# Kernel optimization log

Measured on AMD Instinct MI355X. Metric: run time of the kernel, lower is better.

## Reference

```python
import jax, jax.numpy as jnp
import numpy as np

N = 100000
E = 1600000
IN_DIM = 128
OUT_DIM = 128
K = 2
LN_EPS = 1e-5


def setup_inputs() -> dict:
    key = jax.random.key(0)
    k1, k2, k3, k4 = jax.random.split(key, 4)
    x = jax.random.normal(k1, (N, IN_DIM), dtype=jnp.float32)
    edge_index = jax.random.randint(k2, (2, E), 0, N, dtype=jnp.int64)
    # LayerNorm params (elementwise affine, torch defaults)
    ln_w = jnp.ones((IN_DIM,), dtype=jnp.float32)
    ln_b = jnp.zeros((IN_DIM,), dtype=jnp.float32)
    # SGConv linear params (torch nn.Linear layout: [out, in])
    bound = 1.0 / np.sqrt(IN_DIM)
    W = jax.random.uniform(k3, (OUT_DIM, IN_DIM), minval=-bound, maxval=bound, dtype=jnp.float32)
    b = jax.random.uniform(k4, (OUT_DIM,), minval=-bound, maxval=bound, dtype=jnp.float32)
    return {"x": x, "edge_index": edge_index, "ln_w": ln_w, "ln_b": ln_b, "W": W, "b": b}


def _layer_norm(x, w, b):
    mu = jnp.mean(x, axis=-1, keepdims=True)
    var = jnp.mean(jnp.square(x - mu), axis=-1, keepdims=True)
    return (x - mu) * jax.lax.rsqrt(var + LN_EPS) * w + b


def _sgc_propagate(x, edge_index):
    # gcn_norm with added self-loops: A_hat = D^{-1/2} (A + I) D^{-1/2}
    src, dst = edge_index[0], edge_index[1]
    loop = jnp.arange(N, dtype=src.dtype)
    src_a = jnp.concatenate([src, loop])
    dst_a = jnp.concatenate([dst, loop])
    deg = jax.ops.segment_sum(jnp.ones((E + N,), dtype=x.dtype), dst_a, num_segments=N)
    dinv = jnp.where(deg > 0, jax.lax.rsqrt(jnp.maximum(deg, 1e-12)), 0.0)
    w = dinv[src_a] * dinv[dst_a]  # [E+N]
    for _ in range(K):
        x = jax.ops.segment_sum(x[src_a] * w[:, None], dst_a, num_segments=N)
    return x


def reference(x, edge_index, ln_w, ln_b, W, b):
    y = _layer_norm(x, ln_w, ln_b)
    y = _sgc_propagate(y, edge_index)
    return y @ W.T + b
```

## Files before the change

kernel.cpp:

```cpp
#include <hip/hip_runtime.h>
#include <hip/hip_fp16.h>

#define DIM 128
#define BKT_SHIFT 8
#define BKT_NODES 256
#define CHUNK 8192
#define MAXBUK 1024

typedef _Float16 half8 __attribute__((ext_vector_type(8)));
typedef float f32x4 __attribute__((ext_vector_type(4)));


__global__ __launch_bounds__(256) void k_s1_hist(const int* __restrict__ ei, int* __restrict__ H,
                                                 int E, int NBUK, int NBLK) {
    __shared__ int hist[MAXBUK];
    int b = blockIdx.x, tid = threadIdx.x;
    for (int i = tid; i < NBUK; i += 256) hist[i] = 0;
    __syncthreads();
    int e0 = b * CHUNK, e1 = min(e0 + CHUNK, E);
    for (int e = e0 + tid; e < e1; e += 256) {
        int dst = ei[E + e];
        atomicAdd(&hist[dst >> BKT_SHIFT], 1);
    }
    __syncthreads();
    for (int k = tid; k < NBUK; k += 256) H[(size_t)k * NBLK + b] = hist[k];
}


__global__ __launch_bounds__(256) void k_scanA(const int* __restrict__ in, int* __restrict__ tmp,
                                               int* __restrict__ bsum, int n) {
    __shared__ int s[256];
    int tid = threadIdx.x;
    int i = blockIdx.x * 256 + tid;
    int v = (i < n) ? in[i] : 0;
    s[tid] = v;
    __syncthreads();
    for (int off = 1; off < 256; off <<= 1) {
        int t = (tid >= off) ? s[tid - off] : 0;
        __syncthreads();
        s[tid] += t;
        __syncthreads();
    }
    if (i < n) tmp[i] = s[tid];
    if (tid == 255) bsum[blockIdx.x] = s[255];
}

__global__ __launch_bounds__(1024) void k_scanB(int* __restrict__ bsum, int nb) {
    __shared__ int s[1024];
    int tid = threadIdx.x;
    int v = (tid < nb) ? bsum[tid] : 0;
    s[tid] = v;
    __syncthreads();
    for (int off = 1; off < 1024; off <<= 1) {
        int t = (tid >= off) ? s[tid - off] : 0;
        __syncthreads();
        s[tid] += t;
        __syncthreads();
    }
    if (tid < nb) bsum[tid] = s[tid] - v;
}

__global__ __launch_bounds__(256) void k_scanE(int* __restrict__ H, const int* __restrict__ tmp,
                                               const int* __restrict__ bsum, int n) {
    int i = blockIdx.x * 256 + threadIdx.x;
    if (i < n) H[i] = bsum[blockIdx.x] + tmp[i] - H[i];
}


__global__ __launch_bounds__(256) void k_s3_scatter(const int* __restrict__ ei,
                                                    const int* __restrict__ H,
                                                    int* __restrict__ ssrc,
                                                    unsigned char* __restrict__ sdst, int E,
                                                    int NBUK, int NBLK) {
    __shared__ int off[MAXBUK];
    int b = blockIdx.x, tid = threadIdx.x;
    for (int k = tid; k < NBUK; k += 256) off[k] = H[(size_t)k * NBLK + b];
    __syncthreads();
    int e0 = b * CHUNK, e1 = min(e0 + CHUNK, E);
    for (int e = e0 + tid; e < e1; e += 256) {
        int src = ei[e];
        int dst = ei[E + e];
        int p = atomicAdd(&off[dst >> BKT_SHIFT], 1);
        ssrc[p] = src;
        sdst[p] = (unsigned char)(dst & (BKT_NODES - 1));
    }
}


__global__ __launch_bounds__(256) void k_s4_build(const int* __restrict__ H,
                                                  const int* __restrict__ ssrc,
                                                  const unsigned char* __restrict__ sdst,
                                                  int* __restrict__ rp, float* __restrict__ dinv,
                                                  int* __restrict__ col, int N, int E, int NBUK,
                                                  int NBLK) {
    __shared__ int cnt[BKT_NODES];
    __shared__ int pos[BKT_NODES];
    __shared__ int s[BKT_NODES];
    int bkt = blockIdx.x, tid = threadIdx.x;
    int base = H[(size_t)bkt * NBLK];
    int endv = (bkt + 1 < NBUK) ? H[(size_t)(bkt + 1) * NBLK] : E;
    int m = endv - base;
    cnt[tid] = 0;
    __syncthreads();
    for (int i = tid; i < m; i += 256) atomicAdd(&cnt[sdst[base + i]], 1);
    __syncthreads();
    int v = cnt[tid];
    s[tid] = v;
    __syncthreads();
    for (int off = 1; off < 256; off <<= 1) {
        int t = (tid >= off) ? s[tid - off] : 0;
        __syncthreads();
        s[tid] += t;
        __syncthreads();
    }
    int excl = s[tid] - v;
    pos[tid] = excl;
    int node = bkt * BKT_NODES + tid;
    if (node < N) {
        rp[node] = base + excl;
        dinv[node] = rsqrtf((float)(v + 1));
    }
    __syncthreads();
    for (int i = tid; i < m; i += 256) {
        int r = atomicAdd(&pos[sdst[base + i]], 1);
        col[base + r] = ssrc[base + i];
    }
    if (bkt == 0 && tid == 0) rp[N] = E;
}


__global__ __launch_bounds__(256) void k_ln(const float* __restrict__ x,
                                            const float* __restrict__ w,
                                            const float* __restrict__ bb,
                                            const float* __restrict__ dinv,
                                            __half2* __restrict__ u, int N) {
    int row = (blockIdx.x * 256 + threadIdx.x) >> 6;
    int lane = threadIdx.x & 63;
    if (row >= N) return;
    float2 v = *(const float2*)(x + (size_t)row * DIM + lane * 2);
    float s = v.x + v.y;
#pragma unroll
    for (int o = 32; o; o >>= 1) s += __shfl_xor(s, o, 64);
    float mu = s * (1.0f / 128.0f);
    float dx0 = v.x - mu, dx1 = v.y - mu;
    float ss = dx0 * dx0 + dx1 * dx1;
#pragma unroll
    for (int o = 32; o; o >>= 1) ss += __shfl_xor(ss, o, 64);
    float rs = rsqrtf(ss * (1.0f / 128.0f) + 1e-5f);
    float2 wv = *(const float2*)(w + lane * 2);
    float2 bv = *(const float2*)(bb + lane * 2);
    float di = dinv[row];
    float o0 = (dx0 * rs * wv.x + bv.x) * di;
    float o1 = (dx1 * rs * wv.y + bv.y) * di;
    u[(size_t)row * 64 + lane] = __floats2half2_rn(o0, o1);
}


__global__ __launch_bounds__(256) void k_prop(const _Float16* __restrict__ X,
                                              _Float16* __restrict__ Y,
                                              const int* __restrict__ rp,
                                              const int* __restrict__ col,
                                              const float* __restrict__ dinv, int N, int squared) {
    int tid = threadIdx.x;
    int node = blockIdx.x * 16 + (tid >> 4);
    int q = tid & 15;
    if (node >= N) return;
    const _Float16* xq = X + q * 8;
    half8 selfv = *(const half8*)(xq + (size_t)node * DIM);
    int e0 = rp[node], e1 = rp[node + 1];
    float acc[8];
#pragma unroll
    for (int f = 0; f < 8; f++) acc[f] = 0.f;
    int e = e0;
    for (; e + 7 < e1; e += 8) {
        int s0 = col[e + 0], s1 = col[e + 1], s2 = col[e + 2], s3 = col[e + 3];
        int s4 = col[e + 4], s5 = col[e + 5], s6 = col[e + 6], s7 = col[e + 7];
        half8 g0 = *(const half8*)(xq + (size_t)s0 * DIM);
        half8 g1 = *(const half8*)(xq + (size_t)s1 * DIM);
        half8 g2 = *(const half8*)(xq + (size_t)s2 * DIM);
        half8 g3 = *(const half8*)(xq + (size_t)s3 * DIM);
        half8 g4 = *(const half8*)(xq + (size_t)s4 * DIM);
        half8 g5 = *(const half8*)(xq + (size_t)s5 * DIM);
        half8 g6 = *(const half8*)(xq + (size_t)s6 * DIM);
        half8 g7 = *(const half8*)(xq + (size_t)s7 * DIM);
#pragma unroll
        for (int f = 0; f < 8; f++)
            acc[f] += (((float)g0[f] + (float)g1[f]) + ((float)g2[f] + (float)g3[f])) +
                      (((float)g4[f] + (float)g5[f]) + ((float)g6[f] + (float)g7[f]));
    }
    for (; e + 1 < e1; e += 2) {
        int s0 = col[e], s1 = col[e + 1];
        half8 g0 = *(const half8*)(xq + (size_t)s0 * DIM);
        half8 g1 = *(const half8*)(xq + (size_t)s1 * DIM);
#pragma unroll
        for (int f = 0; f < 8; f++) acc[f] += (float)g0[f] + (float)g1[f];
    }
    if (e < e1) {
        int s = col[e];
        half8 g = *(const half8*)(xq + (size_t)s * DIM);
#pragma unroll
        for (int f = 0; f < 8; f++) acc[f] += (float)g[f];
    }
    float di = dinv[node];
    float sc = squared ? di * di : di;
    half8 o;
#pragma unroll
    for (int f = 0; f < 8; f++) o[f] = (_Float16)(((float)selfv[f] + acc[f]) * sc);
    *(half8*)(Y + (size_t)node * DIM + q * 8) = o;
}


__global__ __launch_bounds__(256) void k_packW(const float* __restrict__ W,
                                               _Float16* __restrict__ pack) {
    int t = blockIdx.x * 256 + threadIdx.x;
    if (t >= 2048) return;
    int lane = t & 63, ks = (t >> 6) & 3, tile = t >> 8;
    int wrow = tile * 16 + (lane & 15);
    int wcol = ks * 32 + 8 * (lane >> 4);
    float4 w0 = *(const float4*)(W + wrow * DIM + wcol);
    float4 w1 = *(const float4*)(W + wrow * DIM + wcol + 4);
    _Float16* dst = pack + (size_t)t * 8;
    dst[0] = (_Float16)w0.x; dst[1] = (_Float16)w0.y;
    dst[2] = (_Float16)w0.z; dst[3] = (_Float16)w0.w;
    dst[4] = (_Float16)w1.x; dst[5] = (_Float16)w1.y;
    dst[6] = (_Float16)w1.z; dst[7] = (_Float16)w1.w;
}

__global__ __launch_bounds__(256) void k_mm(const _Float16* __restrict__ Z,
                                            const _Float16* __restrict__ pack,
                                            const float* __restrict__ bias,
                                            float* __restrict__ out, int N) {
    int wave = threadIdx.x >> 6;
    int lane = threadIdx.x & 63;
    int rB = blockIdx.x * 64 + wave * 16;
    int r = rB + (lane & 15);
    bool rok = (r < N);
    half8 a[4];
    if (rok) {
        const _Float16* zr = Z + (size_t)r * DIM + 8 * (lane >> 4);
#pragma unroll
        for (int ks = 0; ks < 4; ks++) a[ks] = *(const half8*)(zr + ks * 32);
    } else {
#pragma unroll
        for (int ks = 0; ks < 4; ks++)
#pragma unroll
            for (int j = 0; j < 8; j++) a[ks][j] = (_Float16)0;
    }
    int row0 = rB + (lane >> 4) * 4;
#pragma unroll
    for (int tile = 0; tile < 8; tile++) {
        f32x4 d = {0.f, 0.f, 0.f, 0.f};
#pragma unroll
        for (int ks = 0; ks < 4; ks++) {
            half8 bf = *(const half8*)(pack + ((size_t)((tile * 4 + ks) * 64 + lane)) * 8);
            d = __builtin_amdgcn_mfma_f32_16x16x32_f16(a[ks], bf, d, 0, 0, 0);
        }
        int c = tile * 16 + (lane & 15);
        float bv = bias[c];
#pragma unroll
        for (int j = 0; j < 4; j++) {
            int rr = row0 + j;
            if (rr < N) out[(size_t)rr * DIM + c] = d[j] + bv;
        }
    }
}


extern "C" void kernel_launch(void* const* d_in, const int* in_sizes, int n_in, void* d_out,
                              int out_size, void* d_ws, size_t ws_size, hipStream_t stream) {
    const float* x = (const float*)d_in[0];
    const int* ei = (const int*)d_in[1];
    const float* ln_w = (const float*)d_in[2];
    const float* ln_b = (const float*)d_in[3];
    const float* W = (const float*)d_in[4];
    const float* b = (const float*)d_in[5];
    float* out = (float*)d_out;

    int N = in_sizes[0] / DIM;
    int E = in_sizes[1] / 2;

    int NBUK = (N + BKT_NODES - 1) / BKT_NODES;
    int NBLK = (E + CHUNK - 1) / CHUNK;
    int M = NBUK * NBLK;
    int gScan = (M + 255) / 256;

    char* p = (char*)d_ws;
    auto carve = [&](size_t bytes) {
        void* r = (void*)p;
        p += (bytes + 255) & ~(size_t)255;
        return r;
    };
    __half* u0 = (__half*)carve((size_t)N * DIM * 2);
    __half* u1 = (__half*)carve((size_t)N * DIM * 2);
    _Float16* pack = (_Float16*)carve(DIM * DIM * 2);
    int* H = (int*)carve((size_t)M * 4);
    float* dinv = (float*)carve((size_t)N * 4);
    int* rp = (int*)carve((size_t)(N + 1) * 4);
    int* tmp = (int*)carve((size_t)(N > M ? N : M) * 4);
    int* bsum = (int*)carve(1024 * 4);
    int* col = (int*)carve((size_t)E * 4);

    int* ssrc = (int*)u1;
    unsigned char* sdst = (unsigned char*)u1 + ((size_t)E * 4 + 255 & ~(size_t)255);

    int gW = (N + 3) / 4;
    int gP = (N + 15) / 16;
    int gM = (N + 63) / 64;

    k_s1_hist<<<NBLK, 256, 0, stream>>>(ei, H, E, NBUK, NBLK);
    k_scanA<<<gScan, 256, 0, stream>>>(H, tmp, bsum, M);
    k_scanB<<<1, 1024, 0, stream>>>(bsum, gScan);
    k_scanE<<<gScan, 256, 0, stream>>>(H, tmp, bsum, M);
    k_s3_scatter<<<NBLK, 256, 0, stream>>>(ei, H, ssrc, sdst, E, NBUK, NBLK);
    k_s4_build<<<NBUK, 256, 0, stream>>>(H, ssrc, sdst, rp, dinv, col, N, E, NBUK, NBLK);
    k_packW<<<8, 256, 0, stream>>>(W, pack);
    k_ln<<<gW, 256, 0, stream>>>(x, ln_w, ln_b, dinv, (__half2*)u0, N);
    k_prop<<<gP, 256, 0, stream>>>((const _Float16*)u0, (_Float16*)u1, rp, col, dinv, N, 1);
    k_prop<<<gP, 256, 0, stream>>>((const _Float16*)u1, (_Float16*)u0, rp, col, dinv, N, 0);
    k_mm<<<gM, 256, 0, stream>>>((const _Float16*)u0, pack, b, out, N);
}
```

Before: 225.7 us.

## Fuse second propagation with output matmul via LDS tile; enlarge sort blocks

The second SpMM propagation is fused with the final linear layer. Each block aggregates 64 rows into a padded LDS tile and then runs MFMA on that tile, so the fp16 intermediate no longer makes a round trip through global memory and one launch is removed. The histogram and scatter kernels now use 1024-thread blocks on 4096-edge chunks, which gives more blocks and parallelism in preprocessing but also more atomic contention in LDS. Each fused block's four row groups run their gathers serially, which may lower memory-level parallelism compared with the separate prop kernel.

```diff
diff --git a/kernel.cpp b/kernel.cpp
--- a/kernel.cpp
+++ b/kernel.cpp
@@ -4,26 +4,27 @@
 #define DIM 128
 #define BKT_SHIFT 8
 #define BKT_NODES 256
-#define CHUNK 8192
+#define CHUNK 4096
 #define MAXBUK 1024
+#define ZROW 136
 
 typedef _Float16 half8 __attribute__((ext_vector_type(8)));
 typedef float f32x4 __attribute__((ext_vector_type(4)));
 
 
-__global__ __launch_bounds__(256) void k_s1_hist(const int* __restrict__ ei, int* __restrict__ H,
-                                                 int E, int NBUK, int NBLK) {
+__global__ __launch_bounds__(1024) void k_s1_hist(const int* __restrict__ ei, int* __restrict__ H,
+                                                  int E, int NBUK, int NBLK) {
     __shared__ int hist[MAXBUK];
     int b = blockIdx.x, tid = threadIdx.x;
-    for (int i = tid; i < NBUK; i += 256) hist[i] = 0;
+    for (int i = tid; i < NBUK; i += 1024) hist[i] = 0;
     __syncthreads();
     int e0 = b * CHUNK, e1 = min(e0 + CHUNK, E);
-    for (int e = e0 + tid; e < e1; e += 256) {
+    for (int e = e0 + tid; e < e1; e += 1024) {
         int dst = ei[E + e];
         atomicAdd(&hist[dst >> BKT_SHIFT], 1);
     }
     __syncthreads();
-    for (int k = tid; k < NBUK; k += 256) H[(size_t)k * NBLK + b] = hist[k];
+    for (int k = tid; k < NBUK; k += 1024) H[(size_t)k * NBLK + b] = hist[k];
 }
 
 
@@ -67,17 +68,17 @@
 }
 
 
-__global__ __launch_bounds__(256) void k_s3_scatter(const int* __restrict__ ei,
-                                                    const int* __restrict__ H,
-                                                    int* __restrict__ ssrc,
-                                                    unsigned char* __restrict__ sdst, int E,
-                                                    int NBUK, int NBLK) {
+__global__ __launch_bounds__(1024) void k_s3_scatter(const int* __restrict__ ei,
+                                                     const int* __restrict__ H,
+                                                     int* __restrict__ ssrc,
+                                                     unsigned char* __restrict__ sdst, int E,
+                                                     int NBUK, int NBLK) {
     __shared__ int off[MAXBUK];
     int b = blockIdx.x, tid = threadIdx.x;
-    for (int k = tid; k < NBUK; k += 256) off[k] = H[(size_t)k * NBLK + b];
+    for (int k = tid; k < NBUK; k += 1024) off[k] = H[(size_t)k * NBLK + b];
     __syncthreads();
     int e0 = b * CHUNK, e1 = min(e0 + CHUNK, E);
-    for (int e = e0 + tid; e < e1; e += 256) {
+    for (int e = e0 + tid; e < e1; e += 1024) {
         int src = ei[e];
         int dst = ei[E + e];
         int p = atomicAdd(&off[dst >> BKT_SHIFT], 1);
@@ -160,7 +161,7 @@
                                               _Float16* __restrict__ Y,
                                               const int* __restrict__ rp,
                                               const int* __restrict__ col,
-                                              const float* __restrict__ dinv, int N, int squared) {
+                                              const float* __restrict__ dinv, int N) {
     int tid = threadIdx.x;
     int node = blockIdx.x * 16 + (tid >> 4);
     int q = tid & 15;
@@ -202,7 +203,7 @@
         for (int f = 0; f < 8; f++) acc[f] += (float)g[f];
     }
     float di = dinv[node];
-    float sc = squared ? di * di : di;
+    float sc = di * di;
     half8 o;
 #pragma unroll
     for (int f = 0; f < 8; f++) o[f] = (_Float16)(((float)selfv[f] + acc[f]) * sc);
@@ -226,27 +227,79 @@
     dst[6] = (_Float16)w1.z; dst[7] = (_Float16)w1.w;
 }
 
-__global__ __launch_bounds__(256) void k_mm(const _Float16* __restrict__ Z,
-                                            const _Float16* __restrict__ pack,
-                                            const float* __restrict__ bias,
-                                            float* __restrict__ out, int N) {
-    int wave = threadIdx.x >> 6;
-    int lane = threadIdx.x & 63;
-    int rB = blockIdx.x * 64 + wave * 16;
-    int r = rB + (lane & 15);
-    bool rok = (r < N);
+
+__global__ __launch_bounds__(256) void k_prop_mm(const _Float16* __restrict__ X,
+                                                 const int* __restrict__ rp,
+                                                 const int* __restrict__ col,
+                                                 const float* __restrict__ dinv,
+                                                 const _Float16* __restrict__ pack,
+                                                 const float* __restrict__ bias,
+                                                 float* __restrict__ out, int N) {
+    __shared__ _Float16 Z[64 * ZROW];
+    int tid = threadIdx.x;
+    int rB = blockIdx.x * 64;
+    int g = tid >> 4;
+    int q = tid & 15;
+    const _Float16* xq = X + q * 8;
+#pragma unroll
+    for (int k = 0; k < 4; k++) {
+        int lrow = g * 4 + k;
+        int node = rB + lrow;
+        half8 o;
+        if (node < N) {
+            half8 selfv = *(const half8*)(xq + (size_t)node * DIM);
+            int e0 = rp[node], e1 = rp[node + 1];
+            float acc[8];
+#pragma unroll
+            for (int f = 0; f < 8; f++) acc[f] = 0.f;
+            int e = e0;
+            for (; e + 7 < e1; e += 8) {
+                int s0 = col[e + 0], s1 = col[e + 1], s2 = col[e + 2], s3 = col[e + 3];
+                int s4 = col[e + 4], s5 = col[e + 5], s6 = col[e + 6], s7 = col[e + 7];
+                half8 g0 = *(const half8*)(xq + (size_t)s0 * DIM);
+                half8 g1 = *(const half8*)(xq + (size_t)s1 * DIM);
+                half8 g2 = *(const half8*)(xq + (size_t)s2 * DIM);
+                half8 g3 = *(const half8*)(xq + (size_t)s3 * DIM);
+                half8 g4 = *(const half8*)(xq + (size_t)s4 * DIM);
+                half8 g5 = *(const half8*)(xq + (size_t)s5 * DIM);
+                half8 g6 = *(const half8*)(xq + (size_t)s6 * DIM);
+                half8 g7 = *(const half8*)(xq + (size_t)s7 * DIM);
+#pragma unroll
+                for (int f = 0; f < 8; f++)
+                    acc[f] += (((float)g0[f] + (float)g1[f]) + ((float)g2[f] + (float)g3[f])) +
+                              (((float)g4[f] + (float)g5[f]) + ((float)g6[f] + (float)g7[f]));
+            }
+            for (; e + 1 < e1; e += 2) {
+                int s0 = col[e], s1 = col[e + 1];
+                half8 g0 = *(const half8*)(xq + (size_t)s0 * DIM);
+                half8 g1 = *(const half8*)(xq + (size_t)s1 * DIM);
+#pragma unroll
+                for (int f = 0; f < 8; f++) acc[f] += (float)g0[f] + (float)g1[f];
+            }
+            if (e < e1) {
+                int s = col[e];
+                half8 gg = *(const half8*)(xq + (size_t)s * DIM);
+#pragma unroll
+                for (int f = 0; f < 8; f++) acc[f] += (float)gg[f];
+            }
+            float sc = dinv[node];
+#pragma unroll
+            for (int f = 0; f < 8; f++) o[f] = (_Float16)(((float)selfv[f] + acc[f]) * sc);
+        } else {
+#pragma unroll
+            for (int f = 0; f < 8; f++) o[f] = (_Float16)0;
+        }
+        *(half8*)(&Z[lrow * ZROW + q * 8]) = o;
+    }
+    __syncthreads();
+    int wave = tid >> 6;
+    int lane = tid & 63;
+    int rw = wave * 16;
     half8 a[4];
-    if (rok) {
-        const _Float16* zr = Z + (size_t)r * DIM + 8 * (lane >> 4);
-#pragma unroll
-        for (int ks = 0; ks < 4; ks++) a[ks] = *(const half8*)(zr + ks * 32);
-    } else {
-#pragma unroll
-        for (int ks = 0; ks < 4; ks++)
-#pragma unroll
-            for (int j = 0; j < 8; j++) a[ks][j] = (_Float16)0;
-    }
-    int row0 = rB + (lane >> 4) * 4;
+#pragma unroll
+    for (int ks = 0; ks < 4; ks++)
+        a[ks] = *(const half8*)(&Z[(rw + (lane & 15)) * ZROW + ks * 32 + (lane >> 4) * 8]);
+    int row0 = rB + rw + (lane >> 4) * 4;
 #pragma unroll
     for (int tile = 0; tile < 8; tile++) {
         f32x4 d = {0.f, 0.f, 0.f, 0.f};
@@ -307,15 +360,14 @@
     int gP = (N + 15) / 16;
     int gM = (N + 63) / 64;
 
-    k_s1_hist<<<NBLK, 256, 0, stream>>>(ei, H, E, NBUK, NBLK);
+    k_s1_hist<<<NBLK, 1024, 0, stream>>>(ei, H, E, NBUK, NBLK);
     k_scanA<<<gScan, 256, 0, stream>>>(H, tmp, bsum, M);
     k_scanB<<<1, 1024, 0, stream>>>(bsum, gScan);
     k_scanE<<<gScan, 256, 0, stream>>>(H, tmp, bsum, M);
-    k_s3_scatter<<<NBLK, 256, 0, stream>>>(ei, H, ssrc, sdst, E, NBUK, NBLK);
+    k_s3_scatter<<<NBLK, 1024, 0, stream>>>(ei, H, ssrc, sdst, E, NBUK, NBLK);
     k_s4_build<<<NBUK, 256, 0, stream>>>(H, ssrc, sdst, rp, dinv, col, N, E, NBUK, NBLK);
     k_packW<<<8, 256, 0, stream>>>(W, pack);
     k_ln<<<gW, 256, 0, stream>>>(x, ln_w, ln_b, dinv, (__half2*)u0, N);
-    k_prop<<<gP, 256, 0, stream>>>((const _Float16*)u0, (_Float16*)u1, rp, col, dinv, N, 1);
-    k_prop<<<gP, 256, 0, stream>>>((const _Float16*)u1, (_Float16*)u0, rp, col, dinv, N, 0);
-    k_mm<<<gM, 256, 0, stream>>>((const _Float16*)u0, pack, b, out, N);
-}
+    k_prop<<<gP, 256, 0, stream>>>((const _Float16*)u0, (_Float16*)u1, rp, col, dinv, N);
+    k_prop_mm<<<gM, 256, 0, stream>>>((const _Float16*)u1, rp, col, dinv, pack, b, out, N);
+}
```

Result: faster. 219.5 us (-2.7%).

## Pack edge src/dst into one word, fold scan fixup and W packing into build

Applied to the files above, without the earlier changes.

The separate scan-finalise kernel is removed: the exclusive offsets are now computed on the fly from the scan temporaries in the scatter and build kernels. Source and local destination are packed into one 32-bit word, so the sort stage uses a single store and load instead of an int array plus a byte array. W packing is merged into the build kernel as extra blocks. The histogram and scatter kernels now use 1024-thread blocks with smaller chunks. Together these cut launches and memory traffic in the CSR build, but they assume node ids fit in 17 bits.

```diff
diff --git a/kernel.cpp b/kernel.cpp
--- a/kernel.cpp
+++ b/kernel.cpp
@@ -4,26 +4,28 @@
 #define DIM 128
 #define BKT_SHIFT 8
 #define BKT_NODES 256
-#define CHUNK 8192
+#define CHUNK 4096
 #define MAXBUK 1024
+#define SRC_BITS 17
+#define SRC_MASK 0x1FFFF
 
 typedef _Float16 half8 __attribute__((ext_vector_type(8)));
 typedef float f32x4 __attribute__((ext_vector_type(4)));
 
 
-__global__ __launch_bounds__(256) void k_s1_hist(const int* __restrict__ ei, int* __restrict__ H,
-                                                 int E, int NBUK, int NBLK) {
+__global__ __launch_bounds__(1024) void k_s1_hist(const int* __restrict__ ei, int* __restrict__ H,
+                                                  int E, int NBUK, int NBLK) {
     __shared__ int hist[MAXBUK];
     int b = blockIdx.x, tid = threadIdx.x;
-    for (int i = tid; i < NBUK; i += 256) hist[i] = 0;
+    for (int i = tid; i < NBUK; i += 1024) hist[i] = 0;
     __syncthreads();
     int e0 = b * CHUNK, e1 = min(e0 + CHUNK, E);
-    for (int e = e0 + tid; e < e1; e += 256) {
+    for (int e = e0 + tid; e < e1; e += 1024) {
         int dst = ei[E + e];
         atomicAdd(&hist[dst >> BKT_SHIFT], 1);
     }
     __syncthreads();
-    for (int k = tid; k < NBUK; k += 256) H[(size_t)k * NBLK + b] = hist[k];
+    for (int k = tid; k < NBUK; k += 1024) H[(size_t)k * NBLK + b] = hist[k];
 }
 
 
@@ -60,49 +62,67 @@
     if (tid < nb) bsum[tid] = s[tid] - v;
 }
 
-__global__ __launch_bounds__(256) void k_scanE(int* __restrict__ H, const int* __restrict__ tmp,
-                                               const int* __restrict__ bsum, int n) {
-    int i = blockIdx.x * 256 + threadIdx.x;
-    if (i < n) H[i] = bsum[blockIdx.x] + tmp[i] - H[i];
-}
-
-
-__global__ __launch_bounds__(256) void k_s3_scatter(const int* __restrict__ ei,
-                                                    const int* __restrict__ H,
-                                                    int* __restrict__ ssrc,
-                                                    unsigned char* __restrict__ sdst, int E,
-                                                    int NBUK, int NBLK) {
+__device__ __forceinline__ int h_excl(const int* H, const int* tmp, const int* bsum, int i) {
+    return bsum[i >> 8] + tmp[i] - H[i];
+}
+
+
+__global__ __launch_bounds__(1024) void k_s3_scatter(const int* __restrict__ ei,
+                                                     const int* __restrict__ H,
+                                                     const int* __restrict__ tmp,
+                                                     const int* __restrict__ bsum,
+                                                     unsigned int* __restrict__ sedge, int E,
+                                                     int NBUK, int NBLK) {
     __shared__ int off[MAXBUK];
     int b = blockIdx.x, tid = threadIdx.x;
-    for (int k = tid; k < NBUK; k += 256) off[k] = H[(size_t)k * NBLK + b];
+    for (int k = tid; k < NBUK; k += 1024) {
+        int i = k * NBLK + b;
+        off[k] = h_excl(H, tmp, bsum, i);
+    }
     __syncthreads();
     int e0 = b * CHUNK, e1 = min(e0 + CHUNK, E);
-    for (int e = e0 + tid; e < e1; e += 256) {
+    for (int e = e0 + tid; e < e1; e += 1024) {
         int src = ei[e];
         int dst = ei[E + e];
         int p = atomicAdd(&off[dst >> BKT_SHIFT], 1);
-        ssrc[p] = src;
-        sdst[p] = (unsigned char)(dst & (BKT_NODES - 1));
+        sedge[p] = (unsigned int)src | ((unsigned int)(dst & (BKT_NODES - 1)) << SRC_BITS);
     }
 }
 
 
 __global__ __launch_bounds__(256) void k_s4_build(const int* __restrict__ H,
-                                                  const int* __restrict__ ssrc,
-                                                  const unsigned char* __restrict__ sdst,
+                                                  const int* __restrict__ tmp,
+                                                  const int* __restrict__ bsum,
+                                                  const unsigned int* __restrict__ sedge,
                                                   int* __restrict__ rp, float* __restrict__ dinv,
-                                                  int* __restrict__ col, int N, int E, int NBUK,
-                                                  int NBLK) {
+                                                  int* __restrict__ col,
+                                                  const float* __restrict__ W,
+                                                  _Float16* __restrict__ pack, int N, int E,
+                                                  int NBUK, int NBLK) {
+    int bkt = blockIdx.x, tid = threadIdx.x;
+    if (bkt >= NBUK) {
+        int t = (bkt - NBUK) * 256 + tid;
+        int lane = t & 63, ks = (t >> 6) & 3, tile = t >> 8;
+        int wrow = tile * 16 + (lane & 15);
+        int wcol = ks * 32 + 8 * (lane >> 4);
+        float4 w0 = *(const float4*)(W + wrow * DIM + wcol);
+        float4 w1 = *(const float4*)(W + wrow * DIM + wcol + 4);
+        _Float16* dst = pack + (size_t)t * 8;
+        dst[0] = (_Float16)w0.x; dst[1] = (_Float16)w0.y;
+        dst[2] = (_Float16)w0.z; dst[3] = (_Float16)w0.w;
+        dst[4] = (_Float16)w1.x; dst[5] = (_Float16)w1.y;
+        dst[6] = (_Float16)w1.z; dst[7] = (_Float16)w1.w;
+        return;
+    }
     __shared__ int cnt[BKT_NODES];
     __shared__ int pos[BKT_NODES];
     __shared__ int s[BKT_NODES];
-    int bkt = blockIdx.x, tid = threadIdx.x;
-    int base = H[(size_t)bkt * NBLK];
-    int endv = (bkt + 1 < NBUK) ? H[(size_t)(bkt + 1) * NBLK] : E;
+    int base = h_excl(H, tmp, bsum, bkt * NBLK);
+    int endv = (bkt + 1 < NBUK) ? h_excl(H, tmp, bsum, (bkt + 1) * NBLK) : E;
     int m = endv - base;
     cnt[tid] = 0;
     __syncthreads();
-    for (int i = tid; i < m; i += 256) atomicAdd(&cnt[sdst[base + i]], 1);
+    for (int i = tid; i < m; i += 256) atomicAdd(&cnt[sedge[base + i] >> SRC_BITS], 1);
     __syncthreads();
     int v = cnt[tid];
     s[tid] = v;
@@ -122,8 +142,9 @@
     }
     __syncthreads();
     for (int i = tid; i < m; i += 256) {
-        int r = atomicAdd(&pos[sdst[base + i]], 1);
-        col[base + r] = ssrc[base + i];
+        unsigned int ev = sedge[base + i];
+        int r = atomicAdd(&pos[ev >> SRC_BITS], 1);
+        col[base + r] = (int)(ev & SRC_MASK);
     }
     if (bkt == 0 && tid == 0) rp[N] = E;
 }
@@ -209,22 +230,6 @@
     *(half8*)(Y + (size_t)node * DIM + q * 8) = o;
 }
 
-
-__global__ __launch_bounds__(256) void k_packW(const float* __restrict__ W,
-                                               _Float16* __restrict__ pack) {
-    int t = blockIdx.x * 256 + threadIdx.x;
-    if (t >= 2048) return;
-    int lane = t & 63, ks = (t >> 6) & 3, tile = t >> 8;
-    int wrow = tile * 16 + (lane & 15);
-    int wcol = ks * 32 + 8 * (lane >> 4);
-    float4 w0 = *(const float4*)(W + wrow * DIM + wcol);
-    float4 w1 = *(const float4*)(W + wrow * DIM + wcol + 4);
-    _Float16* dst = pack + (size_t)t * 8;
-    dst[0] = (_Float16)w0.x; dst[1] = (_Float16)w0.y;
-    dst[2] = (_Float16)w0.z; dst[3] = (_Float16)w0.w;
-    dst[4] = (_Float16)w1.x; dst[5] = (_Float16)w1.y;
-    dst[6] = (_Float16)w1.z; dst[7] = (_Float16)w1.w;
-}
 
 __global__ __launch_bounds__(256) void k_mm(const _Float16* __restrict__ Z,
                                             const _Float16* __restrict__ pack,
@@ -300,20 +305,18 @@
     int* bsum = (int*)carve(1024 * 4);
     int* col = (int*)carve((size_t)E * 4);
 
-    int* ssrc = (int*)u1;
-    unsigned char* sdst = (unsigned char*)u1 + ((size_t)E * 4 + 255 & ~(size_t)255);
+    unsigned int* sedge = (unsigned int*)u1;
 
     int gW = (N + 3) / 4;
     int gP = (N + 15) / 16;
     int gM = (N + 63) / 64;
 
-    k_s1_hist<<<NBLK, 256, 0, stream>>>(ei, H, E, NBUK, NBLK);
+    k_s1_hist<<<NBLK, 1024, 0, stream>>>(ei, H, E, NBUK, NBLK);
     k_scanA<<<gScan, 256, 0, stream>>>(H, tmp, bsum, M);
     k_scanB<<<1, 1024, 0, stream>>>(bsum, gScan);
-    k_scanE<<<gScan, 256, 0, stream>>>(H, tmp, bsum, M);
-    k_s3_scatter<<<NBLK, 256, 0, stream>>>(ei, H, ssrc, sdst, E, NBUK, NBLK);
-    k_s4_build<<<NBUK, 256, 0, stream>>>(H, ssrc, sdst, rp, dinv, col, N, E, NBUK, NBLK);
-    k_packW<<<8, 256, 0, stream>>>(W, pack);
+    k_s3_scatter<<<NBLK, 1024, 0, stream>>>(ei, H, tmp, bsum, sedge, E, NBUK, NBLK);
+    k_s4_build<<<NBUK + 8, 256, 0, stream>>>(H, tmp, bsum, sedge, rp, dinv, col, W, pack, N, E,
+                                             NBUK, NBLK);
     k_ln<<<gW, 256, 0, stream>>>(x, ln_w, ln_b, dinv, (__half2*)u0, N);
     k_prop<<<gP, 256, 0, stream>>>((const _Float16*)u0, (_Float16*)u1, rp, col, dinv, N, 1);
     k_prop<<<gP, 256, 0, stream>>>((const _Float16*)u1, (_Float16*)u0, rp, col, dinv, N, 0);
```

Result: faster. 204.2 us (-9.5%).
